# Kernel tuning notes

Hardware: AMD Instinct MI355X
Metric: run time of the kernel (lower is better)

## Reference

```python
import jax, jax.numpy as jnp
import numpy as np

SL = 10   # seq_len hard-coded in rearrange
H = 20    # hidden size hard-coded in nn.LSTM
I = 128   # input_size
B = 32768 # batch


def setup_inputs() -> dict:
    key = jax.random.key(0)
    ks = jax.random.split(key, 9)
    k = 1.0 / np.sqrt(H)  # PyTorch LSTM init range
    u = lambda kk, shp: jax.random.uniform(kk, shp, jnp.float32, -k, k)
    return {
        "x": jax.random.normal(ks[0], (B * SL, I), jnp.float32),
        # gate order (PyTorch): i, f, g, o stacked along first dim (4H)
        "W_ih_f": u(ks[1], (4 * H, I)),
        "W_hh_f": u(ks[2], (4 * H, H)),
        "b_ih_f": u(ks[3], (4 * H,)),
        "b_hh_f": u(ks[4], (4 * H,)),
        "W_ih_b": u(ks[5], (4 * H, I)),
        "W_hh_b": u(ks[6], (4 * H, H)),
        "b_ih_b": u(ks[7], (4 * H,)),
        "b_hh_b": u(ks[8], (4 * H,)),
    }


def _lstm_scan(xp, W_hh):
    # xp: [T, B, 4H] precomputed input projection (+biases); returns hs [T, B, H]
    Bn = xp.shape[1]
    h0 = jnp.zeros((Bn, H), xp.dtype)
    c0 = jnp.zeros((Bn, H), xp.dtype)

    def step(carry, xt):
        h, c = carry
        g = xt + h @ W_hh.T
        i, f, gg, o = jnp.split(g, 4, axis=-1)
        i = jax.nn.sigmoid(i)
        f = jax.nn.sigmoid(f)
        gg = jnp.tanh(gg)
        o = jax.nn.sigmoid(o)
        c = f * c + i * gg
        h = o * jnp.tanh(c)
        return (h, c), h

    _, hs = jax.lax.scan(step, (h0, c0), xp)
    return hs


def reference(x, W_ih_f, W_hh_f, b_ih_f, b_hh_f, W_ih_b, W_hh_b, b_ih_b, b_hh_b):
    xb = x.reshape(-1, SL, I)  # '(b sl) i -> b sl i', sl=10
    # forward direction
    xp_f = jnp.einsum('bti,gi->tbg', xb, W_ih_f) + b_ih_f + b_hh_f
    hs_f = _lstm_scan(xp_f, W_hh_f)                     # [T,B,H]
    # backward direction: process reversed sequence
    xp_b = jnp.einsum('bti,gi->tbg', xb[:, ::-1], W_ih_b) + b_ih_b + b_hh_b
    hs_b = _lstm_scan(xp_b, W_hh_b)                     # [T,B,H] (reversed time order)
    # out = lstm_out[:, -1, :] : fwd hidden at t=SL-1 is hs_f[-1];
    # bwd hidden at original t=SL-1 is the FIRST reverse step, hs_b[0].
    return jnp.concatenate([hs_f[-1], hs_b[0]], axis=-1)  # [B, 2H]
```

## Files before the change

kernel.cpp:

```cpp
#include <hip/hip_runtime.h>

#define SL 10
#define NI 128

typedef float f32x4 __attribute__((ext_vector_type(4)));
typedef unsigned int u32;
typedef u32 u32x4 __attribute__((ext_vector_type(4)));
typedef _Float16 h8 __attribute__((ext_vector_type(8)));

__device__ __forceinline__ f32x4 MFH(h8 a, h8 b, f32x4 c){
  return __builtin_amdgcn_mfma_f32_16x16x32_f16(a, b, c, 0, 0, 0);
}
__device__ __forceinline__ float sigf(float x){ return __fdividef(1.f, 1.f + __expf(-x)); }
__device__ __forceinline__ float tanhf2(float x){ return __fdividef(2.f, 1.f + __expf(-2.f*x)) - 1.f; }

__device__ __forceinline__ h8 to_h8(float4 a, float4 b){
  h8 r;
  r[0]=(_Float16)a.x; r[1]=(_Float16)a.y; r[2]=(_Float16)a.z; r[3]=(_Float16)a.w;
  r[4]=(_Float16)b.x; r[5]=(_Float16)b.y; r[6]=(_Float16)b.z; r[7]=(_Float16)b.w;
  return r;
}

__global__ __launch_bounds__(64, 2) void bilstm_kernel(
    const float* __restrict__ x,
    const float* __restrict__ Wih_f, const float* __restrict__ Whh_f,
    const float* __restrict__ bih_f, const float* __restrict__ bhh_f,
    const float* __restrict__ Wih_b,
    const float* __restrict__ bih_b, const float* __restrict__ bhh_b,
    float* __restrict__ out)
{
  __shared__ u32 HB[16*33];
  const int lane = threadIdx.x;
  const int lr = lane & 15;
  const int lg = lane >> 4;
  const long row = (long)blockIdx.x*16 + lr;
  const int gb = (lr&3)*20 + (lr>>2);

  for(int i=lane;i<16*33;i+=64) HB[i]=0;

  h8 WIH[20];
  #pragma unroll
  for(int p=0;p<20;p++){
    const int nt=p>>2, ks=p&3;
    const float* s = Wih_f + (gb+nt*4)*NI + ks*32 + lg*8;
    WIH[p] = to_h8(*(const float4*)s, *(const float4*)(s+4));
  }
  h8 WHH[5];
  #pragma unroll
  for(int nt=0;nt<5;nt++){
    h8 r;
    #pragma unroll
    for(int j=0;j<8;j++){
      const int k = lg*8+j;
      r[j] = (_Float16)((k<20) ? Whh_f[(gb+nt*4)*20+k] : 0.f);
    }
    WHH[nt]=r;
  }
  f32x4 biasv[5];
  #pragma unroll
  for(int nt=0;nt<5;nt++)
    #pragma unroll
    for(int ty=0;ty<4;ty++)
      biasv[nt][ty] = bih_f[ty*20+nt*4+lg] + bhh_f[ty*20+nt*4+lg];

  const float* xbase = x + row*(SL*NI) + lg*8;
  float4 xa[4], xb4[4];
  #pragma unroll
  for(int ks=0;ks<4;ks++){
    xa[ks]  = *(const float4*)(xbase + ks*32);
    xb4[ks] = *(const float4*)(xbase + ks*32 + 4);
  }

  float cst[5]={0.f,0.f,0.f,0.f,0.f};
  h8 bx[4];
  f32x4 acc[5];

  #pragma unroll
  for(int t=0;t<SL;t++){
    #pragma unroll
    for(int ks=0;ks<4;ks++) bx[ks]=to_h8(xa[ks],xb4[ks]);
    if(t+1<SL){
      #pragma unroll
      for(int ks=0;ks<4;ks++){
        xa[ks]  = *(const float4*)(xbase + (t+1)*NI + ks*32);
        xb4[ks] = *(const float4*)(xbase + (t+1)*NI + ks*32 + 4);
      }
    }
    u32x4 hb0, hb1;
    if(t>0){
      const u32* hp = HB + lr*33 + lg*8;
      hb0=*(const u32x4*)hp; hb1=*(const u32x4*)(hp+4);
    }
    #pragma unroll
    for(int nt=0;nt<5;nt++) acc[nt]=biasv[nt];
    #pragma unroll
    for(int ks=0;ks<4;ks++)
      #pragma unroll
      for(int nt=0;nt<5;nt++)
        acc[nt]=MFH(WIH[nt*4+ks], bx[ks], acc[nt]);
    if(t>0){
      u32x4 hh, hl;
      hh[0]=(hb0[0]>>16)|(hb0[1]&0xffff0000u);
      hh[1]=(hb0[2]>>16)|(hb0[3]&0xffff0000u);
      hh[2]=(hb1[0]>>16)|(hb1[1]&0xffff0000u);
      hh[3]=(hb1[2]>>16)|(hb1[3]&0xffff0000u);
      hl[0]=(hb0[0]&0xffffu)|(hb0[1]<<16);
      hl[1]=(hb0[2]&0xffffu)|(hb0[3]<<16);
      hl[2]=(hb1[0]&0xffffu)|(hb1[1]<<16);
      hl[3]=(hb1[2]&0xffffu)|(hb1[3]<<16);
      h8 fh=__builtin_bit_cast(h8,hh), fl=__builtin_bit_cast(h8,hl);
      #pragma unroll
      for(int nt=0;nt<5;nt++){
        acc[nt]=MFH(WHH[nt], fh, acc[nt]);
        acc[nt]=MFH(WHH[nt], fl, acc[nt]);
      }
    }
    #pragma unroll
    for(int nt=0;nt<5;nt++){
      float ig=sigf(acc[nt][0]);
      float fg=sigf(acc[nt][1]);
      float gg=tanhf2(acc[nt][2]);
      float og=sigf(acc[nt][3]);
      cst[nt]=fg*cst[nt]+ig*gg;
      float hv=og*tanhf2(cst[nt]);
      if(t==SL-1){
        out[row*40 + nt*4+lg] = hv;
      } else {
        _Float16 hh16=(_Float16)hv;
        _Float16 hl16=(_Float16)(hv-(float)hh16);
        HB[lr*33 + nt*4+lg] = ((u32)__builtin_bit_cast(unsigned short,hh16)<<16)
                              | (u32)__builtin_bit_cast(unsigned short,hl16);
      }
    }
  }

  f32x4 acc2[5];
  #pragma unroll
  for(int nt=0;nt<5;nt++)
    #pragma unroll
    for(int ty=0;ty<4;ty++)
      acc2[nt][ty] = bih_b[ty*20+nt*4+lg] + bhh_b[ty*20+nt*4+lg];
  #pragma unroll
  for(int ks=0;ks<4;ks++){
    #pragma unroll
    for(int nt=0;nt<5;nt++){
      const float* s = Wih_b + (gb+nt*4)*NI + ks*32 + lg*8;
      acc2[nt]=MFH(to_h8(*(const float4*)s, *(const float4*)(s+4)), bx[ks], acc2[nt]);
    }
  }
  #pragma unroll
  for(int nt=0;nt<5;nt++){
    float ig=sigf(acc2[nt][0]);
    float gg=tanhf2(acc2[nt][2]);
    float og=sigf(acc2[nt][3]);
    out[row*40 + 20 + nt*4+lg] = og*tanhf2(ig*gg);
  }
}

extern "C" void kernel_launch(void* const* d_in, const int* in_sizes, int n_in,
                              void* d_out, int out_size, void* d_ws, size_t ws_size,
                              hipStream_t stream) {
  const float* x     = (const float*)d_in[0];
  const float* Wih_f = (const float*)d_in[1];
  const float* Whh_f = (const float*)d_in[2];
  const float* bih_f = (const float*)d_in[3];
  const float* bhh_f = (const float*)d_in[4];
  const float* Wih_b = (const float*)d_in[5];
  const float* bih_b = (const float*)d_in[7];
  const float* bhh_b = (const float*)d_in[8];
  float* out = (float*)d_out;
  bilstm_kernel<<<dim3(2048), dim3(64), 0, stream>>>(
      x, Wih_f, Whh_f, bih_f, bhh_f, Wih_b, bih_b, bhh_b, out);
}
```

Measured before the change: 52.64 us.

## Double-buffer x loads two steps ahead and prefetch backward weights into buffers

Global loads of x are now prefetched two timesteps ahead using two alternating float4 register buffers. The freed buffers in the last two steps are reused to prefetch the backward-direction W_ih slices, and the backward GEMM loop is software-pipelined over those buffers. The bias is stored as fp16 to save registers, and the Whh load is vectorized. Each change targets global-load latency on the serial recurrence, at the cost of higher register pressure and a small precision loss in the forward bias.

After: 54.50 us. +3.5%, slower.

```diff
diff --git a/kernel.cpp b/kernel.cpp
--- a/kernel.cpp
+++ b/kernel.cpp
@@ -7,6 +7,7 @@
 typedef unsigned int u32;
 typedef u32 u32x4 __attribute__((ext_vector_type(4)));
 typedef _Float16 h8 __attribute__((ext_vector_type(8)));
+typedef _Float16 h4 __attribute__((ext_vector_type(4)));
 
 __device__ __forceinline__ f32x4 MFH(h8 a, h8 b, f32x4 c){
   return __builtin_amdgcn_mfma_f32_16x16x32_f16(a, b, c, 0, 0, 0);
@@ -19,6 +20,27 @@
   r[0]=(_Float16)a.x; r[1]=(_Float16)a.y; r[2]=(_Float16)a.z; r[3]=(_Float16)a.w;
   r[4]=(_Float16)b.x; r[5]=(_Float16)b.y; r[6]=(_Float16)b.z; r[7]=(_Float16)b.w;
   return r;
+}
+
+__device__ __forceinline__ void ldx8(float4 (&b)[8], const float* p){
+  #pragma unroll
+  for(int ks=0;ks<4;ks++){
+    b[2*ks]   = *(const float4*)(p + ks*32);
+    b[2*ks+1] = *(const float4*)(p + ks*32 + 4);
+  }
+}
+__device__ __forceinline__ void ldw4(float4 (&b)[8], const float* Wb, int gb, int g, int lg){
+  #pragma unroll
+  for(int f=0;f<4;f++){
+    const int p = g*4+f;
+    const float* s = Wb + (gb + (p>>2)*4)*NI + (p&3)*32 + lg*8;
+    b[2*f]   = *(const float4*)s;
+    b[2*f+1] = *(const float4*)(s+4);
+  }
+}
+__device__ __forceinline__ void cvt4(h8 (&bx)[4], const float4 (&b)[8]){
+  #pragma unroll
+  for(int ks=0;ks<4;ks++) bx[ks] = to_h8(b[2*ks], b[2*ks+1]);
 }
 
 __global__ __launch_bounds__(64, 2) void bilstm_kernel(
@@ -38,6 +60,11 @@
 
   for(int i=lane;i<16*33;i+=64) HB[i]=0;
 
+  float4 b0[8], b1[8];
+  const float* xb = x + row*(long)(SL*NI) + lg*8;
+  ldx8(b0, xb);
+  ldx8(b1, xb + NI);
+
   h8 WIH[20];
   #pragma unroll
   for(int p=0;p<20;p++){
@@ -48,28 +75,18 @@
   h8 WHH[5];
   #pragma unroll
   for(int nt=0;nt<5;nt++){
-    h8 r;
-    #pragma unroll
-    for(int j=0;j<8;j++){
-      const int k = lg*8+j;
-      r[j] = (_Float16)((k<20) ? Whh_f[(gb+nt*4)*20+k] : 0.f);
-    }
-    WHH[nt]=r;
-  }
-  f32x4 biasv[5];
+    const float* s = Whh_f + (gb+nt*4)*20 + lg*8;
+    float4 wa = {0.f,0.f,0.f,0.f}, wc = {0.f,0.f,0.f,0.f};
+    if(lg<3) wa = *(const float4*)s;
+    if(lg<2) wc = *(const float4*)(s+4);
+    WHH[nt] = to_h8(wa, wc);
+  }
+  h4 bp[5];
   #pragma unroll
   for(int nt=0;nt<5;nt++)
     #pragma unroll
     for(int ty=0;ty<4;ty++)
-      biasv[nt][ty] = bih_f[ty*20+nt*4+lg] + bhh_f[ty*20+nt*4+lg];
-
-  const float* xbase = x + row*(SL*NI) + lg*8;
-  float4 xa[4], xb4[4];
-  #pragma unroll
-  for(int ks=0;ks<4;ks++){
-    xa[ks]  = *(const float4*)(xbase + ks*32);
-    xb4[ks] = *(const float4*)(xbase + ks*32 + 4);
-  }
+      bp[nt][ty] = (_Float16)(bih_f[ty*20+nt*4+lg] + bhh_f[ty*20+nt*4+lg]);
 
   float cst[5]={0.f,0.f,0.f,0.f,0.f};
   h8 bx[4];
@@ -77,14 +94,13 @@
 
   #pragma unroll
   for(int t=0;t<SL;t++){
-    #pragma unroll
-    for(int ks=0;ks<4;ks++) bx[ks]=to_h8(xa[ks],xb4[ks]);
-    if(t+1<SL){
-      #pragma unroll
-      for(int ks=0;ks<4;ks++){
-        xa[ks]  = *(const float4*)(xbase + (t+1)*NI + ks*32);
-        xb4[ks] = *(const float4*)(xbase + (t+1)*NI + ks*32 + 4);
-      }
+    if(t&1) cvt4(bx, b1); else cvt4(bx, b0);
+    if(t+2<SL){
+      if(t&1) ldx8(b1, xb+(t+2)*NI); else ldx8(b0, xb+(t+2)*NI);
+    } else if(t==8){
+      ldw4(b0, Wih_b, gb, 0, lg);
+    } else {
+      ldw4(b1, Wih_b, gb, 1, lg);
     }
     u32x4 hb0, hb1;
     if(t>0){
@@ -92,7 +108,10 @@
       hb0=*(const u32x4*)hp; hb1=*(const u32x4*)(hp+4);
     }
     #pragma unroll
-    for(int nt=0;nt<5;nt++) acc[nt]=biasv[nt];
+    for(int nt=0;nt<5;nt++){
+      acc[nt][0]=(float)bp[nt][0]; acc[nt][1]=(float)bp[nt][1];
+      acc[nt][2]=(float)bp[nt][2]; acc[nt][3]=(float)bp[nt][3];
+    }
     #pragma unroll
     for(int ks=0;ks<4;ks++)
       #pragma unroll
@@ -134,25 +153,32 @@
     }
   }
 
-  f32x4 acc2[5];
+  float bb[20];
   #pragma unroll
   for(int nt=0;nt<5;nt++)
     #pragma unroll
     for(int ty=0;ty<4;ty++)
-      acc2[nt][ty] = bih_b[ty*20+nt*4+lg] + bhh_b[ty*20+nt*4+lg];
-  #pragma unroll
-  for(int ks=0;ks<4;ks++){
-    #pragma unroll
-    for(int nt=0;nt<5;nt++){
-      const float* s = Wih_b + (gb+nt*4)*NI + ks*32 + lg*8;
-      acc2[nt]=MFH(to_h8(*(const float4*)s, *(const float4*)(s+4)), bx[ks], acc2[nt]);
-    }
+      bb[nt*4+ty] = bih_b[ty*20+nt*4+lg] + bhh_b[ty*20+nt*4+lg];
+
+  f32x4 a2[5];
+  #pragma unroll
+  for(int nt=0;nt<5;nt++){ f32x4 z={0.f,0.f,0.f,0.f}; a2[nt]=z; }
+
+  h8 wb[4];
+  #pragma unroll
+  for(int g=0;g<5;g++){
+    if(g&1) cvt4(wb, b1); else cvt4(wb, b0);
+    if(g+2<5){
+      if(g&1) ldw4(b1, Wih_b, gb, g+2, lg); else ldw4(b0, Wih_b, gb, g+2, lg);
+    }
+    #pragma unroll
+    for(int ks=0;ks<4;ks++) a2[g]=MFH(wb[ks], bx[ks], a2[g]);
   }
   #pragma unroll
   for(int nt=0;nt<5;nt++){
-    float ig=sigf(acc2[nt][0]);
-    float gg=tanhf2(acc2[nt][2]);
-    float og=sigf(acc2[nt][3]);
+    float ig=sigf(a2[nt][0]+bb[nt*4+0]);
+    float gg=tanhf2(a2[nt][2]+bb[nt*4+2]);
+    float og=sigf(a2[nt][3]+bb[nt*4+3]);
     out[row*40 + 20 + nt*4+lg] = og*tanhf2(ig*gg);
   }
 }
```

## Stage x through LDS with coalesced row-contiguous loads and double buffering

Applied to the files above, without the earlier changes.

Global loads of x change from each lane reading strided 32-byte pieces of its own row to each half-wave reading a contiguous 512-byte timestep row (float4 per lane). The data are converted to fp16 and written to a double-buffered LDS tile in the MFMA operand layout, then read back as h8 fragments. The aim is better load coalescing and fewer scattered memory transactions. In exchange it adds 8KB of shared memory and extra LDS traffic per timestep, and relies on the double buffer rather than an explicit barrier within the single wave.

Result: slower. 55.21 us (+4.9%).

```diff
diff --git a/kernel.cpp b/kernel.cpp
--- a/kernel.cpp
+++ b/kernel.cpp
@@ -7,6 +7,7 @@
 typedef unsigned int u32;
 typedef u32 u32x4 __attribute__((ext_vector_type(4)));
 typedef _Float16 h8 __attribute__((ext_vector_type(8)));
+typedef _Float16 h4 __attribute__((ext_vector_type(4)));
 
 __device__ __forceinline__ f32x4 MFH(h8 a, h8 b, f32x4 c){
   return __builtin_amdgcn_mfma_f32_16x16x32_f16(a, b, c, 0, 0, 0);
@@ -29,14 +30,27 @@
     const float* __restrict__ bih_b, const float* __restrict__ bhh_b,
     float* __restrict__ out)
 {
+  __shared__ __attribute__((aligned(16))) char XT[8192];
   __shared__ u32 HB[16*33];
-  const int lane = threadIdx.x;
-  const int lr = lane & 15;
-  const int lg = lane >> 4;
-  const long row = (long)blockIdx.x*16 + lr;
+
+  const int l  = threadIdx.x;
+  const int lr = l & 15;
+  const int lg = l >> 4;
+  const int rh = l >> 5;
+  const int kq = l & 31;
+  const long b0 = (long)blockIdx.x * 16;
   const int gb = (lr&3)*20 + (lr>>2);
 
-  for(int i=lane;i<16*33;i+=64) HB[i]=0;
+  for(int i=l;i<16*33;i+=64) HB[i]=0;
+
+  const int woff = ((kq>>3)<<10) + rh*64 + (((kq>>1)&3)<<4) + ((kq&1)<<3);
+  const int roff = (lr*4+lg)*16;
+
+  const float* xsrc = x + (b0 + rh)*(long)(SL*NI) + kq*4;
+
+  float4 buf[8];
+  #pragma unroll
+  for(int j=0;j<8;j++) buf[j] = *(const float4*)(xsrc + j*2*SL*NI);
 
   h8 WIH[20];
   #pragma unroll
@@ -63,29 +77,25 @@
     for(int ty=0;ty<4;ty++)
       biasv[nt][ty] = bih_f[ty*20+nt*4+lg] + bhh_f[ty*20+nt*4+lg];
 
-  const float* xbase = x + row*(SL*NI) + lg*8;
-  float4 xa[4], xb4[4];
-  #pragma unroll
-  for(int ks=0;ks<4;ks++){
-    xa[ks]  = *(const float4*)(xbase + ks*32);
-    xb4[ks] = *(const float4*)(xbase + ks*32 + 4);
-  }
-
   float cst[5]={0.f,0.f,0.f,0.f,0.f};
   h8 bx[4];
   f32x4 acc[5];
 
   #pragma unroll
   for(int t=0;t<SL;t++){
+    const int par = (t&1)<<12;
     #pragma unroll
-    for(int ks=0;ks<4;ks++) bx[ks]=to_h8(xa[ks],xb4[ks]);
+    for(int j=0;j<8;j++){
+      float4 v = buf[j];
+      h4 hv; hv[0]=(_Float16)v.x; hv[1]=(_Float16)v.y; hv[2]=(_Float16)v.z; hv[3]=(_Float16)v.w;
+      *(h4*)(XT + par + woff + j*128) = hv;
+    }
     if(t+1<SL){
       #pragma unroll
-      for(int ks=0;ks<4;ks++){
-        xa[ks]  = *(const float4*)(xbase + (t+1)*NI + ks*32);
-        xb4[ks] = *(const float4*)(xbase + (t+1)*NI + ks*32 + 4);
-      }
+      for(int j=0;j<8;j++) buf[j] = *(const float4*)(xsrc + j*2*SL*NI + (t+1)*NI);
     }
+    #pragma unroll
+    for(int ks=0;ks<4;ks++) bx[ks] = *(const h8*)(XT + par + (ks<<10) + roff);
     u32x4 hb0, hb1;
     if(t>0){
       const u32* hp = HB + lr*33 + lg*8;
@@ -124,7 +134,7 @@
       cst[nt]=fg*cst[nt]+ig*gg;
       float hv=og*tanhf2(cst[nt]);
       if(t==SL-1){
-        out[row*40 + nt*4+lg] = hv;
+        out[(b0+lr)*40 + nt*4+lg] = hv;
       } else {
         _Float16 hh16=(_Float16)hv;
         _Float16 hl16=(_Float16)(hv-(float)hh16);
@@ -134,26 +144,26 @@
     }
   }
 
-  f32x4 acc2[5];
+  f32x4 a2[5];
   #pragma unroll
   for(int nt=0;nt<5;nt++)
     #pragma unroll
     for(int ty=0;ty<4;ty++)
-      acc2[nt][ty] = bih_b[ty*20+nt*4+lg] + bhh_b[ty*20+nt*4+lg];
+      a2[nt][ty] = bih_b[ty*20+nt*4+lg] + bhh_b[ty*20+nt*4+lg];
   #pragma unroll
   for(int ks=0;ks<4;ks++){
     #pragma unroll
     for(int nt=0;nt<5;nt++){
       const float* s = Wih_b + (gb+nt*4)*NI + ks*32 + lg*8;
-      acc2[nt]=MFH(to_h8(*(const float4*)s, *(const float4*)(s+4)), bx[ks], acc2[nt]);
+      a2[nt]=MFH(to_h8(*(const float4*)s, *(const float4*)(s+4)), bx[ks], a2[nt]);
     }
   }
   #pragma unroll
   for(int nt=0;nt<5;nt++){
-    float ig=sigf(acc2[nt][0]);
-    float gg=tanhf2(acc2[nt][2]);
-    float og=sigf(acc2[nt][3]);
-    out[row*40 + 20 + nt*4+lg] = og*tanhf2(ig*gg);
+    float ig=sigf(a2[nt][0]);
+    float gg=tanhf2(a2[nt][2]);
+    float og=sigf(a2[nt][3]);
+    out[(b0+lr)*40 + 20 + nt*4+lg] = og*tanhf2(ig*gg);
   }
 }
 
```

## Split each 16-row LSTM tile across two waves with K-split and gate-split

Applied to the files above, without the earlier changes.

Each block now runs two wavefronts. Each wave computes half of the input-projection K dimension (64 of 128), and the partial sums are exchanged through LDS. The recurrent MFMAs and gate nonlinearities are then divided between the waves (3 and 2 hidden tiles). This halves per-wave registers and serial MFMA chains to raise occupancy and shorten the per-step critical path, at the cost of two block barriers per timestep and extra LDS traffic. Biases are stored as fp16 and the backward weights are reloaded into the same registers.

New measurement: 80.28 us. +52.5%, slower.

```diff
diff --git a/kernel.cpp b/kernel.cpp
--- a/kernel.cpp
+++ b/kernel.cpp
@@ -7,6 +7,7 @@
 typedef unsigned int u32;
 typedef u32 u32x4 __attribute__((ext_vector_type(4)));
 typedef _Float16 h8 __attribute__((ext_vector_type(8)));
+typedef _Float16 h4 __attribute__((ext_vector_type(4)));
 
 __device__ __forceinline__ f32x4 MFH(h8 a, h8 b, f32x4 c){
   return __builtin_amdgcn_mfma_f32_16x16x32_f16(a, b, c, 0, 0, 0);
@@ -21,7 +22,7 @@
   return r;
 }
 
-__global__ __launch_bounds__(64, 2) void bilstm_kernel(
+__global__ __launch_bounds__(128, 4) void bilstm_kernel(
     const float* __restrict__ x,
     const float* __restrict__ Wih_f, const float* __restrict__ Whh_f,
     const float* __restrict__ bih_f, const float* __restrict__ bhh_f,
@@ -29,131 +30,187 @@
     const float* __restrict__ bih_b, const float* __restrict__ bhh_b,
     float* __restrict__ out)
 {
-  __shared__ u32 HB[16*33];
-  const int lane = threadIdx.x;
+  __shared__ __attribute__((aligned(16))) f32x4 PX1[64*3];
+  __shared__ __attribute__((aligned(16))) f32x4 PX0[64*2];
+  __shared__ u32 HB[528];
+
+  const int tid  = threadIdx.x;
+  const int kh   = tid >> 6;
+  const int lane = tid & 63;
   const int lr = lane & 15;
   const int lg = lane >> 4;
-  const long row = (long)blockIdx.x*16 + lr;
+  const long b0 = (long)blockIdx.x * 16;
   const int gb = (lr&3)*20 + (lr>>2);
 
-  for(int i=lane;i<16*33;i+=64) HB[i]=0;
-
-  h8 WIH[20];
-  #pragma unroll
-  for(int p=0;p<20;p++){
-    const int nt=p>>2, ks=p&3;
-    const float* s = Wih_f + (gb+nt*4)*NI + ks*32 + lg*8;
+  for(int i=tid;i<528;i+=128) HB[i]=0;
+
+  h8 WIH[10];
+  #pragma unroll
+  for(int p=0;p<10;p++){
+    const int nt=p>>1, ks=p&1;
+    const float* s = Wih_f + (gb+nt*4)*NI + kh*64 + ks*32 + lg*8;
     WIH[p] = to_h8(*(const float4*)s, *(const float4*)(s+4));
   }
-  h8 WHH[5];
-  #pragma unroll
-  for(int nt=0;nt<5;nt++){
+  h8 WHH[3];
+  #pragma unroll
+  for(int i=0;i<3;i++){
+    const int nt = kh ? (i<2 ? 3+i : 4) : i;
     h8 r;
     #pragma unroll
     for(int j=0;j<8;j++){
       const int k = lg*8+j;
       r[j] = (_Float16)((k<20) ? Whh_f[(gb+nt*4)*20+k] : 0.f);
     }
-    WHH[nt]=r;
-  }
-  f32x4 biasv[5];
+    WHH[i]=r;
+  }
+  h4 bp[5];
   #pragma unroll
   for(int nt=0;nt<5;nt++)
     #pragma unroll
     for(int ty=0;ty<4;ty++)
-      biasv[nt][ty] = bih_f[ty*20+nt*4+lg] + bhh_f[ty*20+nt*4+lg];
-
-  const float* xbase = x + row*(SL*NI) + lg*8;
-  float4 xa[4], xb4[4];
-  #pragma unroll
-  for(int ks=0;ks<4;ks++){
-    xa[ks]  = *(const float4*)(xbase + ks*32);
-    xb4[ks] = *(const float4*)(xbase + ks*32 + 4);
-  }
-
-  float cst[5]={0.f,0.f,0.f,0.f,0.f};
-  h8 bx[4];
+      bp[nt][ty] = kh ? (_Float16)0.f
+                      : (_Float16)(bih_f[ty*20+nt*4+lg] + bhh_f[ty*20+nt*4+lg]);
+
+  const float* xb = x + (b0+lr)*(long)(SL*NI) + kh*64 + lg*8;
+  float4 xa0,xc0,xa1,xc1;
+  xa0=*(const float4*)(xb);    xc0=*(const float4*)(xb+4);
+  xa1=*(const float4*)(xb+32); xc1=*(const float4*)(xb+36);
+
+  float cstA=0.f, cstB=0.f, cstC=0.f;
+  h8 bx0, bx1;
   f32x4 acc[5];
 
   #pragma unroll
   for(int t=0;t<SL;t++){
-    #pragma unroll
-    for(int ks=0;ks<4;ks++) bx[ks]=to_h8(xa[ks],xb4[ks]);
+    bx0 = to_h8(xa0,xc0); bx1 = to_h8(xa1,xc1);
     if(t+1<SL){
-      #pragma unroll
-      for(int ks=0;ks<4;ks++){
-        xa[ks]  = *(const float4*)(xbase + (t+1)*NI + ks*32);
-        xb4[ks] = *(const float4*)(xbase + (t+1)*NI + ks*32 + 4);
-      }
-    }
-    u32x4 hb0, hb1;
+      const float* p = xb + (t+1)*NI;
+      xa0=*(const float4*)(p);    xc0=*(const float4*)(p+4);
+      xa1=*(const float4*)(p+32); xc1=*(const float4*)(p+36);
+    }
+    #pragma unroll
+    for(int nt=0;nt<5;nt++){
+      acc[nt][0]=(float)bp[nt][0]; acc[nt][1]=(float)bp[nt][1];
+      acc[nt][2]=(float)bp[nt][2]; acc[nt][3]=(float)bp[nt][3];
+    }
+    #pragma unroll
+    for(int nt=0;nt<5;nt++){
+      acc[nt]=MFH(WIH[nt*2+0], bx0, acc[nt]);
+      acc[nt]=MFH(WIH[nt*2+1], bx1, acc[nt]);
+    }
+    if(kh){ PX1[lane*3+0]=acc[0]; PX1[lane*3+1]=acc[1]; PX1[lane*3+2]=acc[2]; }
+    else  { PX0[lane*2+0]=acc[3]; PX0[lane*2+1]=acc[4]; }
+    __syncthreads();
+    h8 fh, fl;
     if(t>0){
       const u32* hp = HB + lr*33 + lg*8;
-      hb0=*(const u32x4*)hp; hb1=*(const u32x4*)(hp+4);
-    }
-    #pragma unroll
-    for(int nt=0;nt<5;nt++) acc[nt]=biasv[nt];
-    #pragma unroll
-    for(int ks=0;ks<4;ks++)
+      u32x4 hb0=*(const u32x4*)hp, hb1=*(const u32x4*)(hp+4);
+      u32x4 hhv, hlv;
+      hhv[0]=(hb0[0]>>16)|(hb0[1]&0xffff0000u);
+      hhv[1]=(hb0[2]>>16)|(hb0[3]&0xffff0000u);
+      hhv[2]=(hb1[0]>>16)|(hb1[1]&0xffff0000u);
+      hhv[3]=(hb1[2]>>16)|(hb1[3]&0xffff0000u);
+      hlv[0]=(hb0[0]&0xffffu)|(hb0[1]<<16);
+      hlv[1]=(hb0[2]&0xffffu)|(hb0[3]<<16);
+      hlv[2]=(hb1[0]&0xffffu)|(hb1[1]<<16);
+      hlv[3]=(hb1[2]&0xffffu)|(hb1[3]<<16);
+      fh=__builtin_bit_cast(h8,hhv); fl=__builtin_bit_cast(h8,hlv);
+    }
+    if(kh==0){
+      acc[0]+=PX1[lane*3+0]; acc[1]+=PX1[lane*3+1]; acc[2]+=PX1[lane*3+2];
+      if(t>0){
+        #pragma unroll
+        for(int i=0;i<3;i++){
+          acc[i]=MFH(WHH[i], fh, acc[i]);
+          acc[i]=MFH(WHH[i], fl, acc[i]);
+        }
+      }
       #pragma unroll
-      for(int nt=0;nt<5;nt++)
-        acc[nt]=MFH(WIH[nt*4+ks], bx[ks], acc[nt]);
-    if(t>0){
-      u32x4 hh, hl;
-      hh[0]=(hb0[0]>>16)|(hb0[1]&0xffff0000u);
-      hh[1]=(hb0[2]>>16)|(hb0[3]&0xffff0000u);
-      hh[2]=(hb1[0]>>16)|(hb1[1]&0xffff0000u);
-      hh[3]=(hb1[2]>>16)|(hb1[3]&0xffff0000u);
-      hl[0]=(hb0[0]&0xffffu)|(hb0[1]<<16);
-      hl[1]=(hb0[2]&0xffffu)|(hb0[3]<<16);
-      hl[2]=(hb1[0]&0xffffu)|(hb1[1]<<16);
-      hl[3]=(hb1[2]&0xffffu)|(hb1[3]<<16);
-      h8 fh=__builtin_bit_cast(h8,hh), fl=__builtin_bit_cast(h8,hl);
+      for(int i=0;i<3;i++){
+        float ig=sigf(acc[i][0]);
+        float fg=sigf(acc[i][1]);
+        float gg=tanhf2(acc[i][2]);
+        float og=sigf(acc[i][3]);
+        float& cs = (i==0)?cstA:((i==1)?cstB:cstC);
+        cs = fg*cs + ig*gg;
+        float hv = og*tanhf2(cs);
+        if(t==SL-1){
+          out[(b0+lr)*40 + i*4+lg] = hv;
+        } else {
+          _Float16 hh16=(_Float16)hv;
+          _Float16 hl16=(_Float16)(hv-(float)hh16);
+          HB[lr*33 + i*4+lg] = ((u32)__builtin_bit_cast(unsigned short,hh16)<<16)
+                               | (u32)__builtin_bit_cast(unsigned short,hl16);
+        }
+      }
+    } else {
+      acc[3]+=PX0[lane*2+0]; acc[4]+=PX0[lane*2+1];
+      if(t>0){
+        #pragma unroll
+        for(int i=0;i<2;i++){
+          acc[3+i]=MFH(WHH[i], fh, acc[3+i]);
+          acc[3+i]=MFH(WHH[i], fl, acc[3+i]);
+        }
+      }
       #pragma unroll
-      for(int nt=0;nt<5;nt++){
-        acc[nt]=MFH(WHH[nt], fh, acc[nt]);
-        acc[nt]=MFH(WHH[nt], fl, acc[nt]);
-      }
-    }
-    #pragma unroll
-    for(int nt=0;nt<5;nt++){
-      float ig=sigf(acc[nt][0]);
-      float fg=sigf(acc[nt][1]);
-      float gg=tanhf2(acc[nt][2]);
-      float og=sigf(acc[nt][3]);
-      cst[nt]=fg*cst[nt]+ig*gg;
-      float hv=og*tanhf2(cst[nt]);
-      if(t==SL-1){
-        out[row*40 + nt*4+lg] = hv;
-      } else {
-        _Float16 hh16=(_Float16)hv;
-        _Float16 hl16=(_Float16)(hv-(float)hh16);
-        HB[lr*33 + nt*4+lg] = ((u32)__builtin_bit_cast(unsigned short,hh16)<<16)
-                              | (u32)__builtin_bit_cast(unsigned short,hl16);
-      }
-    }
-  }
-
-  f32x4 acc2[5];
-  #pragma unroll
-  for(int nt=0;nt<5;nt++)
-    #pragma unroll
-    for(int ty=0;ty<4;ty++)
-      acc2[nt][ty] = bih_b[ty*20+nt*4+lg] + bhh_b[ty*20+nt*4+lg];
-  #pragma unroll
-  for(int ks=0;ks<4;ks++){
-    #pragma unroll
-    for(int nt=0;nt<5;nt++){
-      const float* s = Wih_b + (gb+nt*4)*NI + ks*32 + lg*8;
-      acc2[nt]=MFH(to_h8(*(const float4*)s, *(const float4*)(s+4)), bx[ks], acc2[nt]);
-    }
-  }
+      for(int i=0;i<2;i++){
+        float ig=sigf(acc[3+i][0]);
+        float fg=sigf(acc[3+i][1]);
+        float gg=tanhf2(acc[3+i][2]);
+        float og=sigf(acc[3+i][3]);
+        float& cs = (i==0)?cstA:cstB;
+        cs = fg*cs + ig*gg;
+        float hv = og*tanhf2(cs);
+        if(t==SL-1){
+          out[(b0+lr)*40 + (3+i)*4+lg] = hv;
+        } else {
+          _Float16 hh16=(_Float16)hv;
+          _Float16 hl16=(_Float16)(hv-(float)hh16);
+          HB[lr*33 + (3+i)*4+lg] = ((u32)__builtin_bit_cast(unsigned short,hh16)<<16)
+                                   | (u32)__builtin_bit_cast(unsigned short,hl16);
+        }
+      }
+    }
+    __syncthreads();
+  }
+
+  #pragma unroll
+  for(int p=0;p<10;p++){
+    const int nt=p>>1, ks=p&1;
+    const float* s = Wih_b + (gb+nt*4)*NI + kh*64 + ks*32 + lg*8;
+    WIH[p] = to_h8(*(const float4*)s, *(const float4*)(s+4));
+  }
+  f32x4 a2[5];
+  #pragma unroll
+  for(int nt=0;nt<5;nt++){ f32x4 z={0.f,0.f,0.f,0.f}; a2[nt]=z; }
   #pragma unroll
   for(int nt=0;nt<5;nt++){
-    float ig=sigf(acc2[nt][0]);
-    float gg=tanhf2(acc2[nt][2]);
-    float og=sigf(acc2[nt][3]);
-    out[row*40 + 20 + nt*4+lg] = og*tanhf2(ig*gg);
+    a2[nt]=MFH(WIH[nt*2+0], bx0, a2[nt]);
+    a2[nt]=MFH(WIH[nt*2+1], bx1, a2[nt]);
+  }
+  if(kh){ PX1[lane*3+0]=a2[0]; PX1[lane*3+1]=a2[1]; PX1[lane*3+2]=a2[2]; }
+  else  { PX0[lane*2+0]=a2[3]; PX0[lane*2+1]=a2[4]; }
+  __syncthreads();
+  if(kh==0){
+    #pragma unroll
+    for(int i=0;i<3;i++){
+      f32x4 v = a2[i] + PX1[lane*3+i];
+      const int u = i*4+lg;
+      float ig=sigf(v[0] + bih_b[u]       + bhh_b[u]);
+      float gg=tanhf2(v[2] + bih_b[40+u]  + bhh_b[40+u]);
+      float og=sigf(v[3] + bih_b[60+u]    + bhh_b[60+u]);
+      out[(b0+lr)*40 + 20 + u] = og*tanhf2(ig*gg);
+    }
+  } else {
+    #pragma unroll
+    for(int i=0;i<2;i++){
+      f32x4 v = a2[3+i] + PX0[lane*2+i];
+      const int u = (3+i)*4+lg;
+      float ig=sigf(v[0] + bih_b[u]       + bhh_b[u]);
+      float gg=tanhf2(v[2] + bih_b[40+u]  + bhh_b[40+u]);
+      float og=sigf(v[3] + bih_b[60+u]    + bhh_b[60+u]);
+      out[(b0+lr)*40 + 20 + u] = og*tanhf2(ig*gg);
+    }
   }
 }
 
@@ -169,6 +226,6 @@
   const float* bih_b = (const float*)d_in[7];
   const float* bhh_b = (const float*)d_in[8];
   float* out = (float*)d_out;
-  bilstm_kernel<<<dim3(2048), dim3(64), 0, stream>>>(
+  bilstm_kernel<<<dim3(2048), dim3(128), 0, stream>>>(
       x, Wih_f, Whh_f, bih_f, bhh_f, Wih_b, bih_b, bhh_b, out);
 }
```
